# Optimization experiments

Measured on AMD Instinct MI355X. Metric: run time of the kernel, lower is better.

Reference implementation:

```python
import jax, jax.numpy as jnp
import numpy as np

N, T, F_IN = 20000, 8, 64
FILTERS, HEADS = 32, 4
E = 320000
LEAKY = 0.2  # PyG GATConv default negative_slope
HID = HEADS * FILTERS  # 128


def setup_inputs() -> dict:
    key = jax.random.key(0)
    ks = jax.random.split(key, 16)
    g = lambda k, shape, scale: jax.random.normal(k, shape, dtype=jnp.float32) * scale
    return {
        "x": g(ks[0], (N, T, F_IN), 1.0),
        "edge_index": jax.random.randint(ks[1], (2, E), 0, N, dtype=jnp.int32),
        # GATConv 1: lin weight, attention vectors (per head), bias
        "W1": g(ks[2], (HID, F_IN), (2.0 / F_IN) ** 0.5),
        "att_src1": g(ks[3], (HEADS, FILTERS), 0.1),
        "att_dst1": g(ks[4], (HEADS, FILTERS), 0.1),
        "b1": jnp.zeros((HID,), jnp.float32),
        # GATConv 2
        "W2": g(ks[5], (HID, HID), (2.0 / HID) ** 0.5),
        "att_src2": g(ks[6], (HEADS, FILTERS), 0.1),
        "att_dst2": g(ks[7], (HEADS, FILTERS), 0.1),
        "b2": jnp.zeros((HID,), jnp.float32),
        # MLP head
        "lw1": g(ks[8], (FILTERS, HID), (2.0 / HID) ** 0.5),
        "lb1": jnp.zeros((FILTERS,), jnp.float32),
        "lw2": g(ks[9], (1, FILTERS), (2.0 / FILTERS) ** 0.5),
        "lb2": jnp.zeros((1,), jnp.float32),
    }


def gat_layer(x, src, dst, W, a_src, a_dst, b):
    """PyG GATConv (concat=True, add_self_loops already applied to src/dst)."""
    h = (x @ W.T).reshape(N, HEADS, FILTERS)          # [N,H,F]
    es = (h * a_src).sum(-1)                          # [N,H] per-node src score
    ed = (h * a_dst).sum(-1)                          # [N,H] per-node dst score
    e = jax.nn.leaky_relu(es[src] + ed[dst], LEAKY)   # [E',H]
    # segment softmax over incoming edges per destination node
    m = jax.ops.segment_max(e, dst, num_segments=N)
    ex = jnp.exp(e - m[dst])
    denom = jax.ops.segment_sum(ex, dst, num_segments=N)
    alpha = ex / (denom[dst] + 1e-16)                 # [E',H]
    out = jax.ops.segment_sum(h[src] * alpha[:, :, None], dst, num_segments=N)
    return out.reshape(N, HID) + b


def reference(x, edge_index, W1, att_src1, att_dst1, b1,
              W2, att_src2, att_dst2, b2, lw1, lb1, lw2, lb2):
    # add self loops (PyG GATConv default add_self_loops=True)
    loop = jnp.arange(N, dtype=edge_index.dtype)
    src = jnp.concatenate([edge_index[0], loop])
    dst = jnp.concatenate([edge_index[1], loop])

    def step(_, x_t):
        h = jax.nn.elu(gat_layer(x_t, src, dst, W1, att_src1, att_dst1, b1))
        # dropout is identity in eval mode
        h = jax.nn.elu(gat_layer(h, src, dst, W2, att_src2, att_dst2, b2))
        h = jax.nn.relu(h @ lw1.T + lb1)
        y = h @ lw2.T + lb2                            # [N,1]
        return None, y

    _, ys = jax.lax.scan(step, None, jnp.transpose(x, (1, 0, 2)))  # scan over T
    return ys  # [T, N, 1] (stacked version of the original list of outputs)
```

## Files before the change

kernel.cpp:

```cpp
#include <hip/hip_runtime.h>

constexpr int cN     = 20000;
constexpr int cT     = 8;
constexpr int cFIN   = 64;
constexpr int cHEADS = 4;
constexpr int cF     = 32;
constexpr int cHID   = 128;
constexpr int cE     = 320000;
constexpr int cET    = cE + cN;
constexpr int cR     = cN * cT;
constexpr float cLEAKY = 0.2f;

typedef __attribute__((ext_vector_type(8))) short bf16x8;
typedef __attribute__((ext_vector_type(4))) float f32x4;

static __device__ __forceinline__ unsigned short f2bfu(float f) {
    unsigned int u;
    __builtin_memcpy(&u, &f, 4);
    u += 0x7FFFu + ((u >> 16) & 1u);
    return (unsigned short)(u >> 16);
}
static __device__ __forceinline__ void unpack2(unsigned int v, float& lo, float& hi) {
    unsigned int ul = v << 16, uh = v & 0xFFFF0000u;
    __builtin_memcpy(&lo, &ul, 4);
    __builtin_memcpy(&hi, &uh, 4);
}
static __device__ __forceinline__ unsigned int pack2(float lo, float hi) {
    unsigned int ul, uh;
    __builtin_memcpy(&ul, &lo, 4);
    __builtin_memcpy(&uh, &hi, 4);
    ul += 0x7FFFu + ((ul >> 16) & 1u);
    uh += 0x7FFFu + ((uh >> 16) & 1u);
    return (ul >> 16) | (uh & 0xFFFF0000u);
}

__global__ void cvt_w_kernel(const float* W1, const float* W2, const float* lw1,
                             unsigned short* W1b, unsigned short* W2b, unsigned short* lw1b) {
    int i = blockIdx.x * 256 + threadIdx.x;
    if (i < cHID * cFIN)                      W1b[i] = f2bfu(W1[i]);
    else if (i < cHID * cFIN + cHID * cHID)   W2b[i - cHID * cFIN] = f2bfu(W2[i - cHID * cFIN]);
    else if (i < cHID * cFIN + cHID * cHID + cF * cHID)
        lw1b[i - cHID * cFIN - cHID * cHID] = f2bfu(lw1[i - cHID * cFIN - cHID * cHID]);
}

__global__ void deg_init_kernel(int* deg) {
    int n = blockIdx.x * blockDim.x + threadIdx.x;
    if (n < cN) deg[n] = 1;
}
__global__ void deg_count_kernel(const int* ei, int* deg) {
    int e = blockIdx.x * blockDim.x + threadIdx.x;
    if (e < cE) atomicAdd(&deg[ei[cE + e]], 1);
}
__global__ void scan_kernel(const int* deg, int* offs, int* cur) {
    __shared__ int lds[256];
    const int CH = 80;
    int tid  = threadIdx.x;
    int base = tid * CH;
    int tot = 0;
    for (int j = 0; j < CH; j++) {
        int idx = base + j;
        if (idx < cN) tot += deg[idx];
    }
    lds[tid] = tot;
    __syncthreads();
    for (int off = 1; off < 256; off <<= 1) {
        int v = (tid >= off) ? lds[tid - off] : 0;
        __syncthreads();
        lds[tid] += v;
        __syncthreads();
    }
    int run = lds[tid] - tot;
    for (int j = 0; j < CH; j++) {
        int idx = base + j;
        if (idx < cN) { offs[idx] = run; cur[idx] = run; run += deg[idx]; }
    }
    if (tid == 255) offs[cN] = lds[255];
}
__global__ void scatter_kernel(const int* ei, int* cur, int* csr) {
    int e = blockIdx.x * blockDim.x + threadIdx.x;
    if (e >= cET) return;
    int s, d;
    if (e < cE) { s = ei[e]; d = ei[cE + e]; }
    else        { s = e - cE; d = s; }
    int pos = atomicAdd(&cur[d], 1);
    csr[pos] = s;
}

__global__ __launch_bounds__(256) void gemm1_fused_kernel(
        const float* __restrict__ x, const unsigned short* __restrict__ W,
        const float* __restrict__ a_src, const float* __restrict__ a_dst,
        unsigned short* __restrict__ hb, float* __restrict__ es, float* __restrict__ ed) {
    __shared__ float hl[64][132];
    int tid  = threadIdx.x;
    int wave = tid >> 6;
    int lane = tid & 63;
    int q    = lane >> 4;
    int mi   = lane & 15;
    int m0   = blockIdx.x * 64 + wave * 16;

    int rho = m0 + mi;
    int t = rho / cN;
    int n = rho - t * cN;
    const float* xr = x + (size_t)n * (cT * cFIN) + t * cFIN;

    bf16x8 afrag[2];
    #pragma unroll
    for (int s = 0; s < 2; s++) {
        float4 v0 = *(const float4*)(xr + s * 32 + q * 8);
        float4 v1 = *(const float4*)(xr + s * 32 + q * 8 + 4);
        bf16x8 f;
        f[0] = (short)f2bfu(v0.x); f[1] = (short)f2bfu(v0.y);
        f[2] = (short)f2bfu(v0.z); f[3] = (short)f2bfu(v0.w);
        f[4] = (short)f2bfu(v1.x); f[5] = (short)f2bfu(v1.y);
        f[6] = (short)f2bfu(v1.z); f[7] = (short)f2bfu(v1.w);
        afrag[s] = f;
    }

    f32x4 acc[8];
    #pragma unroll
    for (int ct = 0; ct < 8; ct++) acc[ct] = (f32x4){0.f, 0.f, 0.f, 0.f};
    #pragma unroll
    for (int ct = 0; ct < 8; ct++) {
        int c = ct * 16 + mi;
        #pragma unroll
        for (int s = 0; s < 2; s++) {
            bf16x8 bfrag = *(const bf16x8*)(W + (size_t)c * cFIN + s * 32 + q * 8);
            acc[ct] = __builtin_amdgcn_mfma_f32_16x16x32_bf16(afrag[s], bfrag, acc[ct], 0, 0, 0);
        }
    }

    #pragma unroll
    for (int ct = 0; ct < 8; ct++)
        #pragma unroll
        for (int r = 0; r < 4; r++)
            hl[wave * 16 + q * 4 + r][ct * 16 + mi] = acc[ct][r];
    __syncthreads();

    {
        int r2 = tid & 63;
        int hd = tid >> 6;
        int rg = blockIdx.x * 64 + r2;
        const float* hr = &hl[r2][hd * cF];
        const float* sa = a_src + hd * cF;
        const float* da = a_dst + hd * cF;
        float s1 = 0.f, s2 = 0.f;
        #pragma unroll 8
        for (int f = 0; f < cF; f++) {
            float hv = hr[f];
            s1 += hv * sa[f];
            s2 += hv * da[f];
        }
        es[rg * cHEADS + hd] = s1;
        ed[rg * cHEADS + hd] = s2;
    }

    size_t base = (size_t)blockIdx.x * 64 * cHID;
    #pragma unroll
    for (int it = 0; it < 8; it++) {
        int g   = tid + it * 256;
        int row = g >> 5;
        int c4  = (g & 31) * 4;
        float4 v = *(const float4*)&hl[row][c4];
        unsigned int p0 = pack2(v.x, v.y), p1 = pack2(v.z, v.w);
        *(uint2*)(hb + base + (size_t)row * cHID + c4) = make_uint2(p0, p1);
    }
}

__global__ __launch_bounds__(256) void gemm2_mfma_kernel(
        const unsigned short* __restrict__ A, const unsigned short* __restrict__ W,
        const float* __restrict__ a_src, const float* __restrict__ a_dst,
        unsigned short* __restrict__ hb, float* __restrict__ es, float* __restrict__ ed) {
    __shared__ float hl[64][132];
    int tid  = threadIdx.x;
    int wave = tid >> 6;
    int lane = tid & 63;
    int q    = lane >> 4;
    int mi   = lane & 15;
    int m0   = blockIdx.x * 64 + wave * 16;

    bf16x8 afrag[4];
    #pragma unroll
    for (int s = 0; s < 4; s++)
        afrag[s] = *(const bf16x8*)(A + (size_t)(m0 + mi) * cHID + s * 32 + q * 8);

    f32x4 acc[8];
    #pragma unroll
    for (int ct = 0; ct < 8; ct++) acc[ct] = (f32x4){0.f, 0.f, 0.f, 0.f};
    #pragma unroll
    for (int ct = 0; ct < 8; ct++) {
        int c = ct * 16 + mi;
        #pragma unroll
        for (int s = 0; s < 4; s++) {
            bf16x8 bfrag = *(const bf16x8*)(W + (size_t)c * cHID + s * 32 + q * 8);
            acc[ct] = __builtin_amdgcn_mfma_f32_16x16x32_bf16(afrag[s], bfrag, acc[ct], 0, 0, 0);
        }
    }

    #pragma unroll
    for (int ct = 0; ct < 8; ct++)
        #pragma unroll
        for (int r = 0; r < 4; r++)
            hl[wave * 16 + q * 4 + r][ct * 16 + mi] = acc[ct][r];
    __syncthreads();

    {
        int r2 = tid & 63;
        int hd = tid >> 6;
        int rg = blockIdx.x * 64 + r2;
        const float* hr = &hl[r2][hd * cF];
        const float* sa = a_src + hd * cF;
        const float* da = a_dst + hd * cF;
        float s1 = 0.f, s2 = 0.f;
        #pragma unroll 8
        for (int f = 0; f < cF; f++) {
            float hv = hr[f];
            s1 += hv * sa[f];
            s2 += hv * da[f];
        }
        es[rg * cHEADS + hd] = s1;
        ed[rg * cHEADS + hd] = s2;
    }

    size_t base = (size_t)blockIdx.x * 64 * cHID;
    #pragma unroll
    for (int it = 0; it < 8; it++) {
        int g   = tid + it * 256;
        int row = g >> 5;
        int c4  = (g & 31) * 4;
        float4 v = *(const float4*)&hl[row][c4];
        unsigned int p0 = pack2(v.x, v.y), p1 = pack2(v.z, v.w);
        *(uint2*)(hb + base + (size_t)row * cHID + c4) = make_uint2(p0, p1);
    }
}

__global__ __launch_bounds__(256) void agg_kernel(
        const unsigned short* __restrict__ hb, const float* __restrict__ es,
        const float* __restrict__ ed,
        const int* __restrict__ offs, const int* __restrict__ csr,
        const float* __restrict__ bias, unsigned short* __restrict__ outb) {
    int b    = blockIdx.x;
    int t    = b & 7;
    int g    = b >> 3;
    int lrow = threadIdx.x >> 4;
    int n    = g * 16 + lrow;
    int j    = threadIdx.x & 15;
    int head = j >> 2;
    int rho  = t * cN + n;
    int s0 = offs[n], s1 = offs[n + 1];
    float edn = ed[(size_t)rho * cHEADS + head];
    const char* hpc = (const char*)(hb + (size_t)t * cN * cHID);
    const char* epc = (const char*)(es + (size_t)t * cN * cHEADS);
    const char* cc  = (const char*)csr;
    unsigned jo = (unsigned)j * 16u;
    unsigned ho = (unsigned)head * 4u;

    float acc[8] = {};
    float den = 0.f;
    int i = s0;
    for (; i + 3 < s1; i += 4) {
        unsigned io = (unsigned)i * 4u;
        int sa = *(const int*)(cc + io);
        int sb = *(const int*)(cc + io + 4u);
        int sc = *(const int*)(cc + io + 8u);
        int sd = *(const int*)(cc + io + 12u);
        uint4 ra = *(const uint4*)(hpc + (((unsigned)sa) << 8) + jo);
        uint4 rb = *(const uint4*)(hpc + (((unsigned)sb) << 8) + jo);
        uint4 rc = *(const uint4*)(hpc + (((unsigned)sc) << 8) + jo);
        uint4 rd = *(const uint4*)(hpc + (((unsigned)sd) << 8) + jo);
        float ea = *(const float*)(epc + (((unsigned)sa) << 4) + ho) + edn;
        float eb = *(const float*)(epc + (((unsigned)sb) << 4) + ho) + edn;
        float ec = *(const float*)(epc + (((unsigned)sc) << 4) + ho) + edn;
        float ee = *(const float*)(epc + (((unsigned)sd) << 4) + ho) + edn;
        ea = (ea >= 0.f) ? ea : cLEAKY * ea;
        eb = (eb >= 0.f) ? eb : cLEAKY * eb;
        ec = (ec >= 0.f) ? ec : cLEAKY * ec;
        ee = (ee >= 0.f) ? ee : cLEAKY * ee;
        float wa = __expf(ea), wb = __expf(eb), wc = __expf(ec), wd = __expf(ee);
        den += wa; den += wb; den += wc; den += wd;
        float lo, hi;
        unpack2(ra.x, lo, hi); acc[0] += wa * lo; acc[1] += wa * hi;
        unpack2(ra.y, lo, hi); acc[2] += wa * lo; acc[3] += wa * hi;
        unpack2(ra.z, lo, hi); acc[4] += wa * lo; acc[5] += wa * hi;
        unpack2(ra.w, lo, hi); acc[6] += wa * lo; acc[7] += wa * hi;
        unpack2(rb.x, lo, hi); acc[0] += wb * lo; acc[1] += wb * hi;
        unpack2(rb.y, lo, hi); acc[2] += wb * lo; acc[3] += wb * hi;
        unpack2(rb.z, lo, hi); acc[4] += wb * lo; acc[5] += wb * hi;
        unpack2(rb.w, lo, hi); acc[6] += wb * lo; acc[7] += wb * hi;
        unpack2(rc.x, lo, hi); acc[0] += wc * lo; acc[1] += wc * hi;
        unpack2(rc.y, lo, hi); acc[2] += wc * lo; acc[3] += wc * hi;
        unpack2(rc.z, lo, hi); acc[4] += wc * lo; acc[5] += wc * hi;
        unpack2(rc.w, lo, hi); acc[6] += wc * lo; acc[7] += wc * hi;
        unpack2(rd.x, lo, hi); acc[0] += wd * lo; acc[1] += wd * hi;
        unpack2(rd.y, lo, hi); acc[2] += wd * lo; acc[3] += wd * hi;
        unpack2(rd.z, lo, hi); acc[4] += wd * lo; acc[5] += wd * hi;
        unpack2(rd.w, lo, hi); acc[6] += wd * lo; acc[7] += wd * hi;
    }
    for (; i < s1; i++) {
        int sa = *(const int*)(cc + (unsigned)i * 4u);
        uint4 ra = *(const uint4*)(hpc + (((unsigned)sa) << 8) + jo);
        float ea = *(const float*)(epc + (((unsigned)sa) << 4) + ho) + edn;
        ea = (ea >= 0.f) ? ea : cLEAKY * ea;
        float wa = __expf(ea);
        den += wa;
        float lo, hi;
        unpack2(ra.x, lo, hi); acc[0] += wa * lo; acc[1] += wa * hi;
        unpack2(ra.y, lo, hi); acc[2] += wa * lo; acc[3] += wa * hi;
        unpack2(ra.z, lo, hi); acc[4] += wa * lo; acc[5] += wa * hi;
        unpack2(ra.w, lo, hi); acc[6] += wa * lo; acc[7] += wa * hi;
    }
    float inv = 1.f / (den + 1e-16f);
    float4 b0 = *(const float4*)(bias + 8 * j);
    float4 b1 = *(const float4*)(bias + 8 * j + 4);
    float r0 = acc[0] * inv + b0.x; r0 = (r0 > 0.f) ? r0 : expm1f(r0);
    float r1 = acc[1] * inv + b0.y; r1 = (r1 > 0.f) ? r1 : expm1f(r1);
    float r2 = acc[2] * inv + b0.z; r2 = (r2 > 0.f) ? r2 : expm1f(r2);
    float r3 = acc[3] * inv + b0.w; r3 = (r3 > 0.f) ? r3 : expm1f(r3);
    float r4 = acc[4] * inv + b1.x; r4 = (r4 > 0.f) ? r4 : expm1f(r4);
    float r5 = acc[5] * inv + b1.y; r5 = (r5 > 0.f) ? r5 : expm1f(r5);
    float r6 = acc[6] * inv + b1.z; r6 = (r6 > 0.f) ? r6 : expm1f(r6);
    float r7 = acc[7] * inv + b1.w; r7 = (r7 > 0.f) ? r7 : expm1f(r7);
    uint4 o;
    o.x = pack2(r0, r1); o.y = pack2(r2, r3); o.z = pack2(r4, r5); o.w = pack2(r6, r7);
    *(uint4*)(outb + (size_t)rho * cHID + 8 * j) = o;
}

__global__ __launch_bounds__(256) void TemporalGAT_20005957665499_kernel(
        const unsigned short* __restrict__ X, const unsigned short* __restrict__ lw1b,
        const float* __restrict__ lb1, const float* __restrict__ lw2,
        const float* __restrict__ lb2, float* __restrict__ out) {
    int tid  = threadIdx.x;
    int wave = tid >> 6;
    int lane = tid & 63;
    int q    = lane >> 4;
    int mi   = lane & 15;
    int m0   = blockIdx.x * 64 + wave * 16;

    bf16x8 afrag[4];
    #pragma unroll
    for (int s = 0; s < 4; s++)
        afrag[s] = *(const bf16x8*)(X + (size_t)(m0 + mi) * cHID + s * 32 + q * 8);

    f32x4 acc[2];
    acc[0] = (f32x4){0.f, 0.f, 0.f, 0.f};
    acc[1] = (f32x4){0.f, 0.f, 0.f, 0.f};
    #pragma unroll
    for (int ct = 0; ct < 2; ct++) {
        int c = ct * 16 + mi;
        #pragma unroll
        for (int s = 0; s < 4; s++) {
            bf16x8 bfrag = *(const bf16x8*)(lw1b + (size_t)c * cHID + s * 32 + q * 8);
            acc[ct] = __builtin_amdgcn_mfma_f32_16x16x32_bf16(afrag[s], bfrag, acc[ct], 0, 0, 0);
        }
    }

    float lb1a = lb1[mi], lb1b_ = lb1[16 + mi];
    float lw2a = lw2[mi], lw2b_ = lw2[16 + mi];
    float l2 = lb2[0];
    #pragma unroll
    for (int r = 0; r < 4; r++) {
        float va = acc[0][r] + lb1a; va = fmaxf(va, 0.f);
        float vb = acc[1][r] + lb1b_; vb = fmaxf(vb, 0.f);
        float v = va * lw2a + vb * lw2b_;
        v += __shfl_xor(v, 1);
        v += __shfl_xor(v, 2);
        v += __shfl_xor(v, 4);
        v += __shfl_xor(v, 8);
        if (mi == 0) out[m0 + q * 4 + r] = v + l2;
    }
}

extern "C" void kernel_launch(void* const* d_in, const int* in_sizes, int n_in,
                              void* d_out, int out_size, void* d_ws, size_t ws_size,
                              hipStream_t stream) {
    const float* x   = (const float*)d_in[0];
    const int*   ei  = (const int*)d_in[1];
    const float* W1  = (const float*)d_in[2];
    const float* as1 = (const float*)d_in[3];
    const float* ad1 = (const float*)d_in[4];
    const float* b1  = (const float*)d_in[5];
    const float* W2  = (const float*)d_in[6];
    const float* as2 = (const float*)d_in[7];
    const float* ad2 = (const float*)d_in[8];
    const float* b2  = (const float*)d_in[9];
    const float* lw1 = (const float*)d_in[10];
    const float* lb1 = (const float*)d_in[11];
    const float* lw2 = (const float*)d_in[12];
    const float* lb2 = (const float*)d_in[13];
    float* out = (float*)d_out;
    (void)in_sizes; (void)n_in; (void)out_size; (void)ws_size;

    char* ws = (char*)d_ws;
    size_t o = 0;
    auto carveN = [&](size_t bytes) { void* p = ws + o; o += (bytes + 255) & ~(size_t)255; return p; };
    unsigned short* hb   = (unsigned short*)carveN((size_t)cR * cHID * 2);
    unsigned short* xb2  = (unsigned short*)carveN((size_t)cR * cHID * 2);
    unsigned short* xb3  = (unsigned short*)carveN((size_t)cR * cHID * 2);
    unsigned short* W1b  = (unsigned short*)carveN((size_t)cHID * cFIN * 2);
    unsigned short* W2b  = (unsigned short*)carveN((size_t)cHID * cHID * 2);
    unsigned short* lw1b = (unsigned short*)carveN((size_t)cF * cHID * 2);
    float* es_buf  = (float*)carveN((size_t)cR * cHEADS * 4);
    float* ed_buf  = (float*)carveN((size_t)cR * cHEADS * 4);
    int*   deg     = (int*)carveN((size_t)cN * 4);
    int*   offs    = (int*)carveN((size_t)(cN + 1) * 4);
    int*   cursor  = (int*)carveN((size_t)cN * 4);
    int*   csr     = (int*)carveN((size_t)cET * 4);

    cvt_w_kernel<<<(cHID * cFIN + cHID * cHID + cF * cHID + 255) / 256, 256, 0, stream>>>(
        W1, W2, lw1, W1b, W2b, lw1b);

    deg_init_kernel<<<(cN + 255) / 256, 256, 0, stream>>>(deg);
    deg_count_kernel<<<(cE + 255) / 256, 256, 0, stream>>>(ei, deg);
    scan_kernel<<<1, 256, 0, stream>>>(deg, offs, cursor);
    scatter_kernel<<<(cET + 255) / 256, 256, 0, stream>>>(ei, cursor, csr);

    gemm1_fused_kernel<<<cR / 64, 256, 0, stream>>>(x, W1b, as1, ad1, hb, es_buf, ed_buf);
    agg_kernel<<<(cN / 16) * cT, 256, 0, stream>>>(hb, es_buf, ed_buf, offs, csr, b1, xb2);
    gemm2_mfma_kernel<<<cR / 64, 256, 0, stream>>>(xb2, W2b, as2, ad2, hb, es_buf, ed_buf);
    agg_kernel<<<(cN / 16) * cT, 256, 0, stream>>>(hb, es_buf, ed_buf, offs, csr, b2, xb3);
    TemporalGAT_20005957665499_kernel<<<cR / 64, 256, 0, stream>>>(xb3, lw1b, lb1, lw2, lb2, out);
}
```

Before: 417.6 us.

## Sort nodes by degree within 64-node groups and give each head a thread

Adds a per-64-node bitonic sort by in-degree, so each agg block processes nodes of similar degree and wavefront divergence from uneven edge counts drops. The agg kernel now maps 4 threads per node, one per head, each loading 64 bytes per edge, instead of 16 threads per node with 16 bytes each. The 4-edge unroll is removed. Fewer threads per node means fewer lanes reading each edge's index and score, but loads per lane get larger and coalescing across a node's row is reduced, which risks lower memory-level parallelism and higher register use.

Measured after the change: 489.4 us. +17.2%, slower.

```diff
diff --git a/kernel.cpp b/kernel.cpp
--- a/kernel.cpp
+++ b/kernel.cpp
@@ -9,6 +9,7 @@
 constexpr int cE     = 320000;
 constexpr int cET    = cE + cN;
 constexpr int cR     = cN * cT;
+constexpr int cNW    = (cN + 63) / 64;
 constexpr float cLEAKY = 0.2f;
 
 typedef __attribute__((ext_vector_type(8))) short bf16x8;
@@ -84,6 +85,25 @@
     else        { s = e - cE; d = s; }
     int pos = atomicAdd(&cur[d], 1);
     csr[pos] = s;
+}
+
+__global__ void perm_sort_kernel(const int* __restrict__ deg, int* __restrict__ perm) {
+    int g    = blockIdx.x;
+    int lane = threadIdx.x;
+    int node = g * 64 + lane;
+    int key  = (node < cN) ? ((deg[node] << 6) | lane) : 0x7FFFFFFF;
+    #pragma unroll
+    for (int k = 2; k <= 64; k <<= 1) {
+        #pragma unroll
+        for (int j = k >> 1; j > 0; j >>= 1) {
+            int other = __shfl_xor(key, j);
+            bool dirUp = ((lane & k) == 0);
+            bool lower = ((lane & j) == 0);
+            int mn = min(key, other), mx = max(key, other);
+            key = (lower == dirUp) ? mn : mx;
+        }
+    }
+    perm[g * 64 + lane] = (key == 0x7FFFFFFF) ? -1 : (g * 64 + (key & 63));
 }
 
 __global__ __launch_bounds__(256) void gemm1_fused_kernel(
@@ -237,91 +257,86 @@
         const unsigned short* __restrict__ hb, const float* __restrict__ es,
         const float* __restrict__ ed,
         const int* __restrict__ offs, const int* __restrict__ csr,
+        const int* __restrict__ perm,
         const float* __restrict__ bias, unsigned short* __restrict__ outb) {
     int b    = blockIdx.x;
     int t    = b & 7;
     int g    = b >> 3;
-    int lrow = threadIdx.x >> 4;
-    int n    = g * 16 + lrow;
-    int j    = threadIdx.x & 15;
-    int head = j >> 2;
-    int rho  = t * cN + n;
-    int s0 = offs[n], s1 = offs[n + 1];
-    float edn = ed[(size_t)rho * cHEADS + head];
+    int lrow = threadIdx.x >> 2;
+    int j    = threadIdx.x & 3;
+    int n    = perm[g * 64 + lrow];
+    bool valid = (n >= 0);
+    int s0 = 0, s1 = 0;
+    if (valid) { s0 = offs[n]; s1 = offs[n + 1]; }
+    int rho  = t * cN + (valid ? n : 0);
+    float edn = valid ? ed[(size_t)rho * cHEADS + j] : 0.f;
     const char* hpc = (const char*)(hb + (size_t)t * cN * cHID);
     const char* epc = (const char*)(es + (size_t)t * cN * cHEADS);
     const char* cc  = (const char*)csr;
-    unsigned jo = (unsigned)j * 16u;
-    unsigned ho = (unsigned)head * 4u;
-
-    float acc[8] = {};
+    unsigned jo = (unsigned)j * 64u;
+    unsigned ho = (unsigned)j * 4u;
+
+    float4 a0 = {0,0,0,0}, a1 = {0,0,0,0}, a2 = {0,0,0,0}, a3 = {0,0,0,0};
+    float4 a4 = {0,0,0,0}, a5 = {0,0,0,0}, a6 = {0,0,0,0}, a7 = {0,0,0,0};
     float den = 0.f;
-    int i = s0;
-    for (; i + 3 < s1; i += 4) {
-        unsigned io = (unsigned)i * 4u;
-        int sa = *(const int*)(cc + io);
-        int sb = *(const int*)(cc + io + 4u);
-        int sc = *(const int*)(cc + io + 8u);
-        int sd = *(const int*)(cc + io + 12u);
-        uint4 ra = *(const uint4*)(hpc + (((unsigned)sa) << 8) + jo);
-        uint4 rb = *(const uint4*)(hpc + (((unsigned)sb) << 8) + jo);
-        uint4 rc = *(const uint4*)(hpc + (((unsigned)sc) << 8) + jo);
-        uint4 rd = *(const uint4*)(hpc + (((unsigned)sd) << 8) + jo);
-        float ea = *(const float*)(epc + (((unsigned)sa) << 4) + ho) + edn;
-        float eb = *(const float*)(epc + (((unsigned)sb) << 4) + ho) + edn;
-        float ec = *(const float*)(epc + (((unsigned)sc) << 4) + ho) + edn;
-        float ee = *(const float*)(epc + (((unsigned)sd) << 4) + ho) + edn;
-        ea = (ea >= 0.f) ? ea : cLEAKY * ea;
-        eb = (eb >= 0.f) ? eb : cLEAKY * eb;
-        ec = (ec >= 0.f) ? ec : cLEAKY * ec;
-        ee = (ee >= 0.f) ? ee : cLEAKY * ee;
-        float wa = __expf(ea), wb = __expf(eb), wc = __expf(ec), wd = __expf(ee);
-        den += wa; den += wb; den += wc; den += wd;
-        float lo, hi;
-        unpack2(ra.x, lo, hi); acc[0] += wa * lo; acc[1] += wa * hi;
-        unpack2(ra.y, lo, hi); acc[2] += wa * lo; acc[3] += wa * hi;
-        unpack2(ra.z, lo, hi); acc[4] += wa * lo; acc[5] += wa * hi;
-        unpack2(ra.w, lo, hi); acc[6] += wa * lo; acc[7] += wa * hi;
-        unpack2(rb.x, lo, hi); acc[0] += wb * lo; acc[1] += wb * hi;
-        unpack2(rb.y, lo, hi); acc[2] += wb * lo; acc[3] += wb * hi;
-        unpack2(rb.z, lo, hi); acc[4] += wb * lo; acc[5] += wb * hi;
-        unpack2(rb.w, lo, hi); acc[6] += wb * lo; acc[7] += wb * hi;
-        unpack2(rc.x, lo, hi); acc[0] += wc * lo; acc[1] += wc * hi;
-        unpack2(rc.y, lo, hi); acc[2] += wc * lo; acc[3] += wc * hi;
-        unpack2(rc.z, lo, hi); acc[4] += wc * lo; acc[5] += wc * hi;
-        unpack2(rc.w, lo, hi); acc[6] += wc * lo; acc[7] += wc * hi;
-        unpack2(rd.x, lo, hi); acc[0] += wd * lo; acc[1] += wd * hi;
-        unpack2(rd.y, lo, hi); acc[2] += wd * lo; acc[3] += wd * hi;
-        unpack2(rd.z, lo, hi); acc[4] += wd * lo; acc[5] += wd * hi;
-        unpack2(rd.w, lo, hi); acc[6] += wd * lo; acc[7] += wd * hi;
-    }
-    for (; i < s1; i++) {
+    for (int i = s0; i < s1; i++) {
         int sa = *(const int*)(cc + (unsigned)i * 4u);
-        uint4 ra = *(const uint4*)(hpc + (((unsigned)sa) << 8) + jo);
+        const char* hrow = hpc + (((unsigned)sa) << 8) + jo;
+        uint4 r0 = *(const uint4*)(hrow);
+        uint4 r1 = *(const uint4*)(hrow + 16);
+        uint4 r2 = *(const uint4*)(hrow + 32);
+        uint4 r3 = *(const uint4*)(hrow + 48);
         float ea = *(const float*)(epc + (((unsigned)sa) << 4) + ho) + edn;
         ea = (ea >= 0.f) ? ea : cLEAKY * ea;
-        float wa = __expf(ea);
-        den += wa;
+        float w = __expf(ea);
+        den += w;
         float lo, hi;
-        unpack2(ra.x, lo, hi); acc[0] += wa * lo; acc[1] += wa * hi;
-        unpack2(ra.y, lo, hi); acc[2] += wa * lo; acc[3] += wa * hi;
-        unpack2(ra.z, lo, hi); acc[4] += wa * lo; acc[5] += wa * hi;
-        unpack2(ra.w, lo, hi); acc[6] += wa * lo; acc[7] += wa * hi;
-    }
-    float inv = 1.f / (den + 1e-16f);
-    float4 b0 = *(const float4*)(bias + 8 * j);
-    float4 b1 = *(const float4*)(bias + 8 * j + 4);
-    float r0 = acc[0] * inv + b0.x; r0 = (r0 > 0.f) ? r0 : expm1f(r0);
-    float r1 = acc[1] * inv + b0.y; r1 = (r1 > 0.f) ? r1 : expm1f(r1);
-    float r2 = acc[2] * inv + b0.z; r2 = (r2 > 0.f) ? r2 : expm1f(r2);
-    float r3 = acc[3] * inv + b0.w; r3 = (r3 > 0.f) ? r3 : expm1f(r3);
-    float r4 = acc[4] * inv + b1.x; r4 = (r4 > 0.f) ? r4 : expm1f(r4);
-    float r5 = acc[5] * inv + b1.y; r5 = (r5 > 0.f) ? r5 : expm1f(r5);
-    float r6 = acc[6] * inv + b1.z; r6 = (r6 > 0.f) ? r6 : expm1f(r6);
-    float r7 = acc[7] * inv + b1.w; r7 = (r7 > 0.f) ? r7 : expm1f(r7);
-    uint4 o;
-    o.x = pack2(r0, r1); o.y = pack2(r2, r3); o.z = pack2(r4, r5); o.w = pack2(r6, r7);
-    *(uint4*)(outb + (size_t)rho * cHID + 8 * j) = o;
+        unpack2(r0.x, lo, hi); a0.x += w * lo; a0.y += w * hi;
+        unpack2(r0.y, lo, hi); a0.z += w * lo; a0.w += w * hi;
+        unpack2(r0.z, lo, hi); a1.x += w * lo; a1.y += w * hi;
+        unpack2(r0.w, lo, hi); a1.z += w * lo; a1.w += w * hi;
+        unpack2(r1.x, lo, hi); a2.x += w * lo; a2.y += w * hi;
+        unpack2(r1.y, lo, hi); a2.z += w * lo; a2.w += w * hi;
+        unpack2(r1.z, lo, hi); a3.x += w * lo; a3.y += w * hi;
+        unpack2(r1.w, lo, hi); a3.z += w * lo; a3.w += w * hi;
+        unpack2(r2.x, lo, hi); a4.x += w * lo; a4.y += w * hi;
+        unpack2(r2.y, lo, hi); a4.z += w * lo; a4.w += w * hi;
+        unpack2(r2.z, lo, hi); a5.x += w * lo; a5.y += w * hi;
+        unpack2(r2.w, lo, hi); a5.z += w * lo; a5.w += w * hi;
+        unpack2(r3.x, lo, hi); a6.x += w * lo; a6.y += w * hi;
+        unpack2(r3.y, lo, hi); a6.z += w * lo; a6.w += w * hi;
+        unpack2(r3.z, lo, hi); a7.x += w * lo; a7.y += w * hi;
+        unpack2(r3.w, lo, hi); a7.z += w * lo; a7.w += w * hi;
+    }
+    if (valid) {
+        float inv = 1.f / (den + 1e-16f);
+        const float* bp = bias + j * 32;
+        float4 b0 = *(const float4*)(bp + 0),  b1 = *(const float4*)(bp + 4);
+        float4 b2 = *(const float4*)(bp + 8),  b3 = *(const float4*)(bp + 12);
+        float4 b4 = *(const float4*)(bp + 16), b5 = *(const float4*)(bp + 20);
+        float4 b6 = *(const float4*)(bp + 24), b7 = *(const float4*)(bp + 28);
+        float v[32];
+        v[0]=a0.x*inv+b0.x; v[1]=a0.y*inv+b0.y; v[2]=a0.z*inv+b0.z; v[3]=a0.w*inv+b0.w;
+        v[4]=a1.x*inv+b1.x; v[5]=a1.y*inv+b1.y; v[6]=a1.z*inv+b1.z; v[7]=a1.w*inv+b1.w;
+        v[8]=a2.x*inv+b2.x; v[9]=a2.y*inv+b2.y; v[10]=a2.z*inv+b2.z; v[11]=a2.w*inv+b2.w;
+        v[12]=a3.x*inv+b3.x; v[13]=a3.y*inv+b3.y; v[14]=a3.z*inv+b3.z; v[15]=a3.w*inv+b3.w;
+        v[16]=a4.x*inv+b4.x; v[17]=a4.y*inv+b4.y; v[18]=a4.z*inv+b4.z; v[19]=a4.w*inv+b4.w;
+        v[20]=a5.x*inv+b5.x; v[21]=a5.y*inv+b5.y; v[22]=a5.z*inv+b5.z; v[23]=a5.w*inv+b5.w;
+        v[24]=a6.x*inv+b6.x; v[25]=a6.y*inv+b6.y; v[26]=a6.z*inv+b6.z; v[27]=a6.w*inv+b6.w;
+        v[28]=a7.x*inv+b7.x; v[29]=a7.y*inv+b7.y; v[30]=a7.z*inv+b7.z; v[31]=a7.w*inv+b7.w;
+        #pragma unroll
+        for (int k = 0; k < 32; k++) v[k] = (v[k] > 0.f) ? v[k] : expm1f(v[k]);
+        unsigned short* orow = outb + (size_t)rho * cHID + j * 32;
+        #pragma unroll
+        for (int k = 0; k < 4; k++) {
+            uint4 o;
+            o.x = pack2(v[k*8+0], v[k*8+1]);
+            o.y = pack2(v[k*8+2], v[k*8+3]);
+            o.z = pack2(v[k*8+4], v[k*8+5]);
+            o.w = pack2(v[k*8+6], v[k*8+7]);
+            *(uint4*)(orow + k * 8) = o;
+        }
+    }
 }
 
 __global__ __launch_bounds__(256) void TemporalGAT_20005957665499_kernel(
@@ -404,6 +419,7 @@
     int*   offs    = (int*)carveN((size_t)(cN + 1) * 4);
     int*   cursor  = (int*)carveN((size_t)cN * 4);
     int*   csr     = (int*)carveN((size_t)cET * 4);
+    int*   perm    = (int*)carveN((size_t)cNW * 64 * 4);
 
     cvt_w_kernel<<<(cHID * cFIN + cHID * cHID + cF * cHID + 255) / 256, 256, 0, stream>>>(
         W1, W2, lw1, W1b, W2b, lw1b);
@@ -412,10 +428,11 @@
     deg_count_kernel<<<(cE + 255) / 256, 256, 0, stream>>>(ei, deg);
     scan_kernel<<<1, 256, 0, stream>>>(deg, offs, cursor);
     scatter_kernel<<<(cET + 255) / 256, 256, 0, stream>>>(ei, cursor, csr);
+    perm_sort_kernel<<<cNW, 64, 0, stream>>>(deg, perm);
 
     gemm1_fused_kernel<<<cR / 64, 256, 0, stream>>>(x, W1b, as1, ad1, hb, es_buf, ed_buf);
-    agg_kernel<<<(cN / 16) * cT, 256, 0, stream>>>(hb, es_buf, ed_buf, offs, csr, b1, xb2);
+    agg_kernel<<<cNW * cT, 256, 0, stream>>>(hb, es_buf, ed_buf, offs, csr, perm, b1, xb2);
     gemm2_mfma_kernel<<<cR / 64, 256, 0, stream>>>(xb2, W2b, as2, ad2, hb, es_buf, ed_buf);
-    agg_kernel<<<(cN / 16) * cT, 256, 0, stream>>>(hb, es_buf, ed_buf, offs, csr, b2, xb3);
+    agg_kernel<<<cNW * cT, 256, 0, stream>>>(hb, es_buf, ed_buf, offs, csr, perm, b2, xb3);
     TemporalGAT_20005957665499_kernel<<<cR / 64, 256, 0, stream>>>(xb3, lw1b, lb1, lw2, lb2, out);
 }
```
